# Kernel tuning notes

Hardware: AMD Instinct MI355X
Metric: run time of the kernel (lower is better)

The kernel has to match this reference:

```python
import jax, jax.numpy as jnp
import numpy as np
from jax import lax

EPS = 1e-5
GROUPS = 8
NUM_HEADS = 8


def setup_inputs() -> dict:
    key = jax.random.key(0)
    ks = jax.random.split(key, 3)
    C = 512
    x = jax.random.normal(ks[0], (8, C, 32, 32), dtype=jnp.float32)
    gamma = jnp.ones((C,), jnp.float32)
    beta = jnp.zeros((C,), jnp.float32)
    w_qkv = jax.random.normal(ks[1], (3 * C, C), dtype=jnp.float32) * (1.0 / np.sqrt(C))
    b_qkv = jnp.zeros((3 * C,), jnp.float32)
    w_proj = jax.random.normal(ks[2], (C, C), dtype=jnp.float32) * (1.0 / np.sqrt(C))
    b_proj = jnp.zeros((C,), jnp.float32)
    return {"x": x, "gamma": gamma, "beta": beta, "w_qkv": w_qkv,
            "b_qkv": b_qkv, "w_proj": w_proj, "b_proj": b_proj}


def reference(x, gamma, beta, w_qkv, b_qkv, w_proj, b_proj):
    b, c, h, w = x.shape
    hd = c // NUM_HEADS
    L = h * w
    # GroupNorm over (c/G, h, w) per group
    xg = x.reshape(b, GROUPS, c // GROUPS, h, w)
    mean = jnp.mean(xg, axis=(2, 3, 4), keepdims=True)
    var = jnp.var(xg, axis=(2, 3, 4), keepdims=True)
    xn = ((xg - mean) * lax.rsqrt(var + EPS)).reshape(b, c, h, w)
    xn = xn * gamma[None, :, None, None] + beta[None, :, None, None]
    # 1x1 conv QKV projection over flattened spatial dim
    xr = xn.reshape(b, c, L)
    qkv = jnp.einsum('oc,bcl->bol', w_qkv, xr) + b_qkv[None, :, None]
    q, k, v = jnp.split(qkv, 3, axis=1)
    # [b, H, L, hd]
    q = q.reshape(b, NUM_HEADS, hd, L).transpose(0, 1, 3, 2)
    k = k.reshape(b, NUM_HEADS, hd, L).transpose(0, 1, 3, 2)
    v = v.reshape(b, NUM_HEADS, hd, L).transpose(0, 1, 3, 2)
    scale = 1.0 / np.sqrt(hd).astype(np.float32)
    attn = jnp.einsum('bhqd,bhkd->bhqk', q, k) * scale
    attn = jax.nn.softmax(attn, axis=-1)
    out = jnp.einsum('bhqk,bhkd->bhqd', attn, v)  # [b, H, L, hd]
    out = out.transpose(0, 1, 3, 2).reshape(b, c, L)
    out = jnp.einsum('oc,bcl->bol', w_proj, out) + b_proj[None, :, None]
    return x + out.reshape(b, c, h, w)
```

## Files before the change

kernel.cpp:

```cpp
#include <hip/hip_runtime.h>
#include <hip/hip_bf16.h>

typedef unsigned short u16;
typedef __attribute__((ext_vector_type(8))) short short8;
typedef __attribute__((ext_vector_type(4))) float floatx4;
typedef __attribute__((ext_vector_type(16))) float floatx16;
typedef __attribute__((ext_vector_type(4))) unsigned uint4v;

struct __attribute__((aligned(8))) u16x4 { u16 x, y, z, w; };
struct __attribute__((aligned(16))) u16x8 { u16 v[8]; };

__device__ __forceinline__ u16 f2bf(float f) {
  unsigned u = __builtin_bit_cast(unsigned, f);
  u += 0x7fff + ((u >> 16) & 1);
  return (u16)(u >> 16);
}

__device__ __forceinline__ unsigned cvt_pk_bf16(float lo, float hi) {
  unsigned d;
  asm("v_cvt_pk_bf16_f32 %0, %1, %2" : "=v"(d) : "v"(lo), "v"(hi));
  return d;
}

__device__ __forceinline__ void gload_lds16(const u16* g, u16* l) {
  __builtin_amdgcn_global_load_lds(
      (const __attribute__((address_space(1))) void*)g,
      (__attribute__((address_space(3))) void*)l, 16, 0, 0);
}

__global__ __launch_bounds__(256) void k_convert(
    const float* __restrict__ wq, const float* __restrict__ wp,
    u16* __restrict__ oq, u16* __restrict__ op) {
  int t = blockIdx.x * 256 + threadIdx.x;
  constexpr int NQ4 = (1536 * 512) / 4;
  constexpr int NP4 = (512 * 512) / 4;
  if (t < NQ4) {
    float4 v = reinterpret_cast<const float4*>(wq)[t];
    u16x4 o = { f2bf(v.x), f2bf(v.y), f2bf(v.z), f2bf(v.w) };
    reinterpret_cast<u16x4*>(oq)[t] = o;
  } else if (t - NQ4 < NP4) {
    int i = t - NQ4;
    float4 v = reinterpret_cast<const float4*>(wp)[i];
    u16x4 o = { f2bf(v.x), f2bf(v.y), f2bf(v.z), f2bf(v.w) };
    reinterpret_cast<u16x4*>(op)[i] = o;
  }
}

__global__ __launch_bounds__(256) void k_gn_stats(const float* __restrict__ x,
                                                  float* __restrict__ stats) {
  int bg = blockIdx.x >> 3, sl = blockIdx.x & 7;
  int b = bg >> 3, g = bg & 7;
  const float* base = x + ((size_t)(b * 512 + g * 64) * 1024) + sl * 128;
  float s = 0.f, ss = 0.f;
#pragma unroll
  for (int i = 0; i < 8; ++i) {
    int idx = threadIdx.x + i * 256;
    int c = idx >> 5, l4 = idx & 31;
    float4 v = *reinterpret_cast<const float4*>(base + (size_t)c * 1024 + l4 * 4);
    s += v.x + v.y + v.z + v.w;
    ss += v.x * v.x + v.y * v.y + v.z * v.z + v.w * v.w;
  }
#pragma unroll
  for (int d = 1; d < 64; d <<= 1) { s += __shfl_xor(s, d); ss += __shfl_xor(ss, d); }
  __shared__ float rs[4], rss[4];
  int wid = threadIdx.x >> 6;
  if ((threadIdx.x & 63) == 0) { rs[wid] = s; rss[wid] = ss; }
  __syncthreads();
  if (threadIdx.x == 0) {
    stats[(bg * 8 + sl) * 2]     = rs[0] + rs[1] + rs[2] + rs[3];
    stats[(bg * 8 + sl) * 2 + 1] = rss[0] + rss[1] + rss[2] + rss[3];
  }
}

__global__ __launch_bounds__(256) void k_gn_norm(
    const float* __restrict__ x, const float* __restrict__ gamma,
    const float* __restrict__ beta, const float* __restrict__ stats,
    u16* __restrict__ xnT) {
  int bg = blockIdx.x >> 3, sl = blockIdx.x & 7;
  int b = bg >> 3, g = bg & 7;
  float s = 0.f, ss = 0.f;
#pragma unroll
  for (int i = 0; i < 8; ++i) { s += stats[(bg * 8 + i) * 2]; ss += stats[(bg * 8 + i) * 2 + 1]; }
  const float inv_n = 1.0f / 65536.0f;
  float mean = s * inv_n;
  float var = ss * inv_n - mean * mean;
  float istd = rsqrtf(var + 1e-5f);
  __shared__ float tile[128 * 65];
  const float* base = x + ((size_t)(b * 512 + g * 64) * 1024) + sl * 128;
#pragma unroll
  for (int i = 0; i < 8; ++i) {
    int idx = threadIdx.x + i * 256;
    int c = idx >> 5, l4 = idx & 31;
    float4 v = *reinterpret_cast<const float4*>(base + (size_t)c * 1024 + l4 * 4);
    float gm = gamma[g * 64 + c];
    float ga = gm * istd;
    float be = beta[g * 64 + c] - mean * ga;
    tile[(l4 * 4 + 0) * 65 + c] = v.x * ga + be;
    tile[(l4 * 4 + 1) * 65 + c] = v.y * ga + be;
    tile[(l4 * 4 + 2) * 65 + c] = v.z * ga + be;
    tile[(l4 * 4 + 3) * 65 + c] = v.w * ga + be;
  }
  __syncthreads();
  u16* obase = xnT + ((size_t)(b * 1024 + sl * 128) * 512) + g * 64;
#pragma unroll
  for (int i = 0; i < 8; ++i) {
    int idx = threadIdx.x + i * 256;
    int l = idx >> 4, c4 = (idx & 15) * 4;
    u16x4 o = { f2bf(tile[l * 65 + c4]),     f2bf(tile[l * 65 + c4 + 1]),
                f2bf(tile[l * 65 + c4 + 2]), f2bf(tile[l * 65 + c4 + 3]) };
    *reinterpret_cast<u16x4*>(obase + (size_t)l * 512 + c4) = o;
  }
}

template <int MODE>
__global__ __launch_bounds__(512) void k_gemm(
    const u16* __restrict__ A, const u16* __restrict__ Bm,
    const float* __restrict__ bias, const float* __restrict__ xres,
    u16* __restrict__ Qb, u16* __restrict__ Kb, u16* __restrict__ Vb,
    float* __restrict__ out) {
  int b = blockIdx.x & 7;
  int rem = blockIdx.x >> 3;
  int mt = rem >> 3, nt = rem & 7;
  int tid = threadIdx.x;
  int lane = tid & 63, wid = tid >> 6;
  int wm = wid >> 2, wn = wid & 3;

  union SM {
    u16 ab[2][2][128 * 64];
    u16 c16[128 * 136];
    float c32[128 * 128];
  };
  __shared__ SM sm;

  floatx4 z = {0.f, 0.f, 0.f, 0.f};
  floatx4 acc[4][2];
#pragma unroll
  for (int m = 0; m < 4; ++m)
#pragma unroll
    for (int n = 0; n < 2; ++n) acc[m][n] = z;

  const u16* Abase = A + (size_t)(mt * 128) * 512;
  const u16* Bbase = Bm + ((size_t)(b * 1024 + nt * 128)) * 512;
  int cb0 = (lane & 7) ^ (lane >> 3);
  const u16* asrc = Abase + (size_t)(wid * 16 + (lane >> 3)) * 512 + cb0 * 8;
  const u16* bsrc = Bbase + (size_t)(wid * 16 + (lane >> 3)) * 512 + cb0 * 8;

#define STAGE(BUF, KK)                                                           \
  {                                                                              \
    _Pragma("unroll")                                                            \
    for (int j = 0; j < 2; ++j) {                                                \
      gload_lds16(asrc + (size_t)j * 8 * 512 + (KK) * 64,                        \
                  &sm.ab[BUF][0][(wid * 16 + j * 8) * 64]);                      \
      gload_lds16(bsrc + (size_t)j * 8 * 512 + (KK) * 64,                        \
                  &sm.ab[BUF][1][(wid * 16 + j * 8) * 64]);                      \
    }                                                                            \
  }

  STAGE(0, 0);
#pragma unroll
  for (int kk = 0; kk < 8; ++kk) {
    const int cur = kk & 1;
    if (kk < 7) {
      STAGE(cur ^ 1, kk + 1);
      asm volatile("s_waitcnt vmcnt(4)" ::: "memory");
    } else {
      asm volatile("s_waitcnt vmcnt(0)" ::: "memory");
    }
    __builtin_amdgcn_s_barrier();
    __builtin_amdgcn_sched_barrier(0);
    const u16* Asc = sm.ab[cur][0];
    const u16* Bsc = sm.ab[cur][1];
#pragma unroll
    for (int kc = 0; kc < 2; ++kc) {
      int cbk = kc * 4 + (lane >> 4);
      short8 af[4], bf[2];
#pragma unroll
      for (int m = 0; m < 4; ++m) {
        int row = wm * 64 + m * 16 + (lane & 15);
        af[m] = *reinterpret_cast<const short8*>(Asc + row * 64 + ((cbk ^ (row & 7)) * 8));
      }
#pragma unroll
      for (int n = 0; n < 2; ++n) {
        int row = wn * 32 + n * 16 + (lane & 15);
        bf[n] = *reinterpret_cast<const short8*>(Bsc + row * 64 + ((cbk ^ (row & 7)) * 8));
      }
      __builtin_amdgcn_s_setprio(1);
#pragma unroll
      for (int m = 0; m < 4; ++m)
#pragma unroll
        for (int n = 0; n < 2; ++n)
          acc[m][n] = __builtin_amdgcn_mfma_f32_16x16x32_bf16(af[m], bf[n], acc[m][n], 0, 0, 0);
      __builtin_amdgcn_s_setprio(0);
    }
    __builtin_amdgcn_s_barrier();
  }
#undef STAGE

  int sec = (MODE == 0) ? (mt >> 2) : 0;
  int ow0 = (mt & 3) * 128;
#pragma unroll
  for (int m = 0; m < 4; ++m) {
#pragma unroll
    for (int n = 0; n < 2; ++n) {
#pragma unroll
      for (int r = 0; r < 4; ++r) {
        int o_l = wm * 64 + m * 16 + ((lane >> 4) * 4) + r;
        int l_l = wn * 32 + n * 16 + (lane & 15);
        float v = acc[m][n][r] + bias[mt * 128 + o_l];
        if (MODE == 0) {
          if (sec == 0) v *= 0.18033688f;
          u16 bv = f2bf(v);
          if (sec < 2) sm.c16[l_l * 136 + o_l] = bv;
          else         sm.c16[o_l * 136 + l_l] = bv;
        } else {
          sm.c32[o_l * 128 + l_l] = v;
        }
      }
    }
  }
  __syncthreads();
  if (MODE == 0) {
    u16* dst = (sec == 0) ? Qb : (sec == 1 ? Kb : Vb);
#pragma unroll
    for (int p = 0; p < 4; ++p) {
      int row = p * 32 + (tid >> 4);
      int col = (tid & 15) * 8;
      u16x8 vv = *reinterpret_cast<const u16x8*>(&sm.c16[row * 136 + col]);
      size_t gi;
      if (sec < 2) gi = ((size_t)(b * 1024 + nt * 128 + row)) * 512 + ow0 + col;
      else         gi = ((size_t)(b * 512 + ow0 + row)) * 1024 + nt * 128 + col;
      *reinterpret_cast<u16x8*>(dst + gi) = vv;
    }
  } else {
#pragma unroll
    for (int p = 0; p < 8; ++p) {
      int row = p * 16 + (tid >> 5);
      int col = (tid & 31) * 4;
      float4 vv = *reinterpret_cast<const float4*>(&sm.c32[row * 128 + col]);
      size_t gi = ((size_t)(b * 512 + mt * 128 + row)) * 1024 + nt * 128 + col;
      float4 xr = *reinterpret_cast<const float4*>(xres + gi);
      vv.x += xr.x; vv.y += xr.y; vv.z += xr.z; vv.w += xr.w;
      *reinterpret_cast<float4*>(out + gi) = vv;
    }
  }
}

__global__ __launch_bounds__(256) void k_attn(
    const u16* __restrict__ Qb, const u16* __restrict__ Kb,
    const u16* __restrict__ Vb, u16* __restrict__ OT) {
  int b = blockIdx.x & 7;
  int h = (blockIdx.x >> 3) & 7;
  int qt = blockIdx.x >> 6;
  int tid = threadIdx.x;
  int lane = tid & 63, wid = tid >> 6;
  int l31 = lane & 31, g = lane >> 5;
  int r7 = l31 & 7;
  __shared__ u16 Ks[64 * 64], Vs[64 * 64];

  short8 qf[4];
  int qrow = qt * 128 + wid * 32 + l31;
  const u16* qp = Qb + ((size_t)(b * 1024 + qrow)) * 512 + h * 64 + g * 8;
#pragma unroll
  for (int kc2 = 0; kc2 < 4; ++kc2)
    qf[kc2] = *reinterpret_cast<const short8*>(qp + kc2 * 16);

  floatx16 oacc[2];
#pragma unroll
  for (int nd = 0; nd < 2; ++nd)
#pragma unroll
    for (int r = 0; r < 16; ++r) oacc[nd][r] = 0.f;
  float m = -1e30f, se = 0.f;

  const u16* ksrc[2]; const u16* vsrc[2]; int sdst[2];
#pragma unroll
  for (int i = 0; i < 2; ++i) {
    int idx = tid + i * 256;
    int row = idx >> 3, cb = idx & 7;
    ksrc[i] = Kb + ((size_t)(b * 1024 + row)) * 512 + h * 64 + cb * 8;
    vsrc[i] = Vb + ((size_t)(b * 512 + h * 64 + row)) * 1024 + cb * 8;
    sdst[i] = row * 64 + ((cb ^ (row & 7)) * 8);
  }
  short8 kreg[2], vreg[2];
#pragma unroll
  for (int i = 0; i < 2; ++i) {
    kreg[i] = *reinterpret_cast<const short8*>(ksrc[i]);
    vreg[i] = *reinterpret_cast<const short8*>(vsrc[i]);
  }

  for (int kt = 0; kt < 16; ++kt) {
#pragma unroll
    for (int i = 0; i < 2; ++i) {
      *reinterpret_cast<short8*>(Ks + sdst[i]) = kreg[i];
      *reinterpret_cast<short8*>(Vs + sdst[i]) = vreg[i];
    }
    __syncthreads();
    if (kt < 15) {
#pragma unroll
      for (int i = 0; i < 2; ++i) {
        kreg[i] = *reinterpret_cast<const short8*>(ksrc[i] + (size_t)(kt + 1) * 64 * 512);
        vreg[i] = *reinterpret_cast<const short8*>(vsrc[i] + (kt + 1) * 64);
      }
    }
    floatx16 sacc[2];
#pragma unroll
    for (int nk = 0; nk < 2; ++nk)
#pragma unroll
      for (int r = 0; r < 16; ++r) sacc[nk][r] = 0.f;
#pragma unroll
    for (int nk = 0; nk < 2; ++nk) {
      const u16* krow = Ks + (nk * 32 + l31) * 64;
#pragma unroll
      for (int kc2 = 0; kc2 < 4; ++kc2) {
        int cb = kc2 * 2 + g;
        short8 kf = *reinterpret_cast<const short8*>(krow + ((cb ^ r7) * 8));
        sacc[nk] = __builtin_amdgcn_mfma_f32_32x32x16_bf16(kf, qf[kc2], sacc[nk], 0, 0, 0);
      }
    }
    float pmax = sacc[0][0];
#pragma unroll
    for (int r = 1; r < 16; ++r) pmax = fmaxf(pmax, sacc[0][r]);
#pragma unroll
    for (int r = 0; r < 16; ++r) pmax = fmaxf(pmax, sacc[1][r]);
    pmax = fmaxf(pmax, __shfl_xor(pmax, 32));
    if (__any(pmax > m + 8.0f)) {
      float mn = fmaxf(m, pmax);
      float f = __builtin_amdgcn_exp2f(m - mn);
      m = mn;
      se *= f;
#pragma unroll
      for (int nd = 0; nd < 2; ++nd)
#pragma unroll
        for (int r = 0; r < 16; ++r) oacc[nd][r] *= f;
    }
    float sum = 0.f;
#pragma unroll
    for (int nk = 0; nk < 2; ++nk)
#pragma unroll
      for (int r = 0; r < 16; ++r) {
        float pv = __builtin_amdgcn_exp2f(sacc[nk][r] - m);
        sacc[nk][r] = pv;
        sum += pv;
      }
    sum += __shfl_xor(sum, 32);
    se += sum;
#pragma unroll
    for (int nk = 0; nk < 2; ++nk) {
#pragma unroll
      for (int kc = 0; kc < 2; ++kc) {
        int base = kc * 8;
        unsigned w0 = cvt_pk_bf16(sacc[nk][base + 0], sacc[nk][base + 1]);
        unsigned w2 = cvt_pk_bf16(sacc[nk][base + 4], sacc[nk][base + 5]);
        auto s0 = __builtin_amdgcn_permlane32_swap((int)w0, (int)w2, false, false);
        unsigned w1 = cvt_pk_bf16(sacc[nk][base + 2], sacc[nk][base + 3]);
        unsigned w3 = cvt_pk_bf16(sacc[nk][base + 6], sacc[nk][base + 7]);
        auto s1 = __builtin_amdgcn_permlane32_swap((int)w1, (int)w3, false, false);
        short8 pf = __builtin_bit_cast(short8,
            uint4v{(unsigned)s0[0], (unsigned)s1[0], (unsigned)s0[1], (unsigned)s1[1]});
#pragma unroll
        for (int nd = 0; nd < 2; ++nd) {
          const u16* vrow = Vs + (nd * 32 + l31) * 64;
          int cb = nk * 4 + kc * 2 + g;
          short8 vf = *reinterpret_cast<const short8*>(vrow + ((cb ^ r7) * 8));
          oacc[nd] = __builtin_amdgcn_mfma_f32_32x32x16_bf16(vf, pf, oacc[nd], 0, 0, 0);
        }
      }
    }
    __syncthreads();
  }
  float inv = 1.0f / se;
  u16* obase = OT + ((size_t)(b * 1024 + qrow)) * 512 + h * 64;
#pragma unroll
  for (int nd = 0; nd < 2; ++nd) {
#pragma unroll
    for (int rq = 0; rq < 4; ++rq) {
      u16x4 o = { f2bf(oacc[nd][rq * 4 + 0] * inv), f2bf(oacc[nd][rq * 4 + 1] * inv),
                  f2bf(oacc[nd][rq * 4 + 2] * inv), f2bf(oacc[nd][rq * 4 + 3] * inv) };
      *reinterpret_cast<u16x4*>(obase + nd * 32 + rq * 8 + g * 4) = o;
    }
  }
}

extern "C" void kernel_launch(void* const* d_in, const int* in_sizes, int n_in,
                              void* d_out, int out_size, void* d_ws, size_t ws_size,
                              hipStream_t stream) {
  const float* x      = (const float*)d_in[0];
  const float* gamma  = (const float*)d_in[1];
  const float* beta   = (const float*)d_in[2];
  const float* w_qkv  = (const float*)d_in[3];
  const float* b_qkv  = (const float*)d_in[4];
  const float* w_proj = (const float*)d_in[5];
  const float* b_proj = (const float*)d_in[6];
  float* out = (float*)d_out;

  char* ws = (char*)d_ws;
  size_t off = 0;
  float* stats = (float*)(ws + off); off += 4096;
  u16* wqb = (u16*)(ws + off); off += (size_t)1536 * 512 * 2;
  u16* wpb = (u16*)(ws + off); off += (size_t)512 * 512 * 2;
  u16* xnT = (u16*)(ws + off); off += (size_t)8 * 1024 * 512 * 2;
  u16* Qb  = (u16*)(ws + off); off += (size_t)8 * 1024 * 512 * 2;
  u16* Kb  = (u16*)(ws + off); off += (size_t)8 * 1024 * 512 * 2;
  u16* Vb  = (u16*)(ws + off); off += (size_t)8 * 1024 * 512 * 2;
  u16* OT  = (u16*)(ws + off); off += (size_t)8 * 1024 * 512 * 2;
  if (ws_size < off) return;

  k_convert<<<1024, 256, 0, stream>>>(w_qkv, w_proj, wqb, wpb);
  k_gn_stats<<<512, 256, 0, stream>>>(x, stats);
  k_gn_norm<<<512, 256, 0, stream>>>(x, gamma, beta, stats, xnT);
  k_gemm<0><<<768, 512, 0, stream>>>(wqb, xnT, b_qkv, nullptr, Qb, Kb, Vb, nullptr);
  k_attn<<<512, 256, 0, stream>>>(Qb, Kb, Vb, OT);
  k_gemm<1><<<256, 512, 0, stream>>>(wpb, OT, b_proj, x, nullptr, nullptr, nullptr, out);
}
```

Before: 85.68 us.

## Split GEMM into dedicated QKV and proj kernels and remap block indices

Separates the templated GEMM into a QKV kernel and a projection kernel. The projection kernel now uses 256 threads with 4x4 MFMA tiles per wave, so each wave does more work per LDS read. Block index decoding in the QKV, attention and projection kernels is reordered so consecutive blocks share the same batch (and head), which is meant to improve L2 locality for shared operands. The trade-off is higher register pressure in the projection kernel and fewer waves per block.

```diff
diff --git a/kernel.cpp b/kernel.cpp
--- a/kernel.cpp
+++ b/kernel.cpp
@@ -112,15 +112,14 @@
   }
 }
 
-template <int MODE>
-__global__ __launch_bounds__(512) void k_gemm(
+__global__ __launch_bounds__(512) void k_qkv(
     const u16* __restrict__ A, const u16* __restrict__ Bm,
-    const float* __restrict__ bias, const float* __restrict__ xres,
-    u16* __restrict__ Qb, u16* __restrict__ Kb, u16* __restrict__ Vb,
-    float* __restrict__ out) {
-  int b = blockIdx.x & 7;
+    const float* __restrict__ bias,
+    u16* __restrict__ Qb, u16* __restrict__ Kb, u16* __restrict__ Vb) {
+  int nt = blockIdx.x & 7;
   int rem = blockIdx.x >> 3;
-  int mt = rem >> 3, nt = rem & 7;
+  int b = rem & 7;
+  int mt = rem >> 3;
   int tid = threadIdx.x;
   int lane = tid & 63, wid = tid >> 6;
   int wm = wid >> 2, wn = wid & 3;
@@ -128,16 +127,14 @@
   union SM {
     u16 ab[2][2][128 * 64];
     u16 c16[128 * 136];
-    float c32[128 * 128];
   };
   __shared__ SM sm;
 
-  floatx4 z = {0.f, 0.f, 0.f, 0.f};
   floatx4 acc[4][2];
 #pragma unroll
   for (int m = 0; m < 4; ++m)
 #pragma unroll
-    for (int n = 0; n < 2; ++n) acc[m][n] = z;
+    for (int n = 0; n < 2; ++n) acc[m][n] = floatx4{0.f, 0.f, 0.f, 0.f};
 
   const u16* Abase = A + (size_t)(mt * 128) * 512;
   const u16* Bbase = Bm + ((size_t)(b * 1024 + nt * 128)) * 512;
@@ -196,7 +193,7 @@
   }
 #undef STAGE
 
-  int sec = (MODE == 0) ? (mt >> 2) : 0;
+  int sec = mt >> 2;
   int ow0 = (mt & 3) * 128;
 #pragma unroll
   for (int m = 0; m < 4; ++m) {
@@ -207,50 +204,137 @@
         int o_l = wm * 64 + m * 16 + ((lane >> 4) * 4) + r;
         int l_l = wn * 32 + n * 16 + (lane & 15);
         float v = acc[m][n][r] + bias[mt * 128 + o_l];
-        if (MODE == 0) {
-          if (sec == 0) v *= 0.18033688f;
-          u16 bv = f2bf(v);
-          if (sec < 2) sm.c16[l_l * 136 + o_l] = bv;
-          else         sm.c16[o_l * 136 + l_l] = bv;
-        } else {
-          sm.c32[o_l * 128 + l_l] = v;
-        }
+        if (sec == 0) v *= 0.18033688f;
+        u16 bv = f2bf(v);
+        if (sec < 2) sm.c16[l_l * 136 + o_l] = bv;
+        else         sm.c16[o_l * 136 + l_l] = bv;
       }
     }
   }
   __syncthreads();
-  if (MODE == 0) {
-    u16* dst = (sec == 0) ? Qb : (sec == 1 ? Kb : Vb);
-#pragma unroll
-    for (int p = 0; p < 4; ++p) {
-      int row = p * 32 + (tid >> 4);
-      int col = (tid & 15) * 8;
-      u16x8 vv = *reinterpret_cast<const u16x8*>(&sm.c16[row * 136 + col]);
-      size_t gi;
-      if (sec < 2) gi = ((size_t)(b * 1024 + nt * 128 + row)) * 512 + ow0 + col;
-      else         gi = ((size_t)(b * 512 + ow0 + row)) * 1024 + nt * 128 + col;
-      *reinterpret_cast<u16x8*>(dst + gi) = vv;
-    }
-  } else {
-#pragma unroll
-    for (int p = 0; p < 8; ++p) {
-      int row = p * 16 + (tid >> 5);
-      int col = (tid & 31) * 4;
-      float4 vv = *reinterpret_cast<const float4*>(&sm.c32[row * 128 + col]);
-      size_t gi = ((size_t)(b * 512 + mt * 128 + row)) * 1024 + nt * 128 + col;
-      float4 xr = *reinterpret_cast<const float4*>(xres + gi);
-      vv.x += xr.x; vv.y += xr.y; vv.z += xr.z; vv.w += xr.w;
-      *reinterpret_cast<float4*>(out + gi) = vv;
-    }
+  u16* dst = (sec == 0) ? Qb : (sec == 1 ? Kb : Vb);
+#pragma unroll
+  for (int p = 0; p < 4; ++p) {
+    int row = p * 32 + (tid >> 4);
+    int col = (tid & 15) * 8;
+    u16x8 vv = *reinterpret_cast<const u16x8*>(&sm.c16[row * 136 + col]);
+    size_t gi;
+    if (sec < 2) gi = ((size_t)(b * 1024 + nt * 128 + row)) * 512 + ow0 + col;
+    else         gi = ((size_t)(b * 512 + ow0 + row)) * 1024 + nt * 128 + col;
+    *reinterpret_cast<u16x8*>(dst + gi) = vv;
+  }
+}
+
+__global__ __launch_bounds__(256) void k_proj(
+    const u16* __restrict__ A, const u16* __restrict__ Bm,
+    const float* __restrict__ bias, const float* __restrict__ xres,
+    float* __restrict__ out) {
+  int nt = blockIdx.x & 7;
+  int rem = blockIdx.x >> 3;
+  int b = rem & 7;
+  int mt = rem >> 3;
+  int tid = threadIdx.x;
+  int lane = tid & 63, wid = tid >> 6;
+  int wm = wid >> 1, wn = wid & 1;
+
+  union SM {
+    u16 ab[2][2][128 * 64];
+    float c32[128 * 128];
+  };
+  __shared__ SM sm;
+
+  floatx4 acc[4][4];
+#pragma unroll
+  for (int m = 0; m < 4; ++m)
+#pragma unroll
+    for (int n = 0; n < 4; ++n) acc[m][n] = floatx4{0.f, 0.f, 0.f, 0.f};
+
+  const u16* Abase = A + (size_t)(mt * 128) * 512;
+  const u16* Bbase = Bm + ((size_t)(b * 1024 + nt * 128)) * 512;
+  int cb0 = (lane & 7) ^ (lane >> 3);
+  const u16* asrc = Abase + (size_t)(wid * 32 + (lane >> 3)) * 512 + cb0 * 8;
+  const u16* bsrc = Bbase + (size_t)(wid * 32 + (lane >> 3)) * 512 + cb0 * 8;
+
+#define PSTAGE(BUF, KK)                                                          \
+  {                                                                              \
+    _Pragma("unroll")                                                            \
+    for (int j = 0; j < 4; ++j) {                                                \
+      gload_lds16(asrc + (size_t)j * 8 * 512 + (KK) * 64,                        \
+                  &sm.ab[BUF][0][(wid * 32 + j * 8) * 64]);                      \
+      gload_lds16(bsrc + (size_t)j * 8 * 512 + (KK) * 64,                        \
+                  &sm.ab[BUF][1][(wid * 32 + j * 8) * 64]);                      \
+    }                                                                            \
+  }
+
+  PSTAGE(0, 0);
+#pragma unroll
+  for (int kk = 0; kk < 8; ++kk) {
+    const int cur = kk & 1;
+    if (kk < 7) {
+      PSTAGE(cur ^ 1, kk + 1);
+      asm volatile("s_waitcnt vmcnt(8)" ::: "memory");
+    } else {
+      asm volatile("s_waitcnt vmcnt(0)" ::: "memory");
+    }
+    __builtin_amdgcn_s_barrier();
+    __builtin_amdgcn_sched_barrier(0);
+    const u16* Asc = sm.ab[cur][0];
+    const u16* Bsc = sm.ab[cur][1];
+#pragma unroll
+    for (int kc = 0; kc < 2; ++kc) {
+      int cbk = kc * 4 + (lane >> 4);
+      short8 af[4], bf[4];
+#pragma unroll
+      for (int m = 0; m < 4; ++m) {
+        int row = wm * 64 + m * 16 + (lane & 15);
+        af[m] = *reinterpret_cast<const short8*>(Asc + row * 64 + ((cbk ^ (row & 7)) * 8));
+      }
+#pragma unroll
+      for (int n = 0; n < 4; ++n) {
+        int row = wn * 64 + n * 16 + (lane & 15);
+        bf[n] = *reinterpret_cast<const short8*>(Bsc + row * 64 + ((cbk ^ (row & 7)) * 8));
+      }
+      __builtin_amdgcn_s_setprio(1);
+#pragma unroll
+      for (int m = 0; m < 4; ++m)
+#pragma unroll
+        for (int n = 0; n < 4; ++n)
+          acc[m][n] = __builtin_amdgcn_mfma_f32_16x16x32_bf16(af[m], bf[n], acc[m][n], 0, 0, 0);
+      __builtin_amdgcn_s_setprio(0);
+    }
+    __builtin_amdgcn_s_barrier();
+  }
+#undef PSTAGE
+
+#pragma unroll
+  for (int m = 0; m < 4; ++m)
+#pragma unroll
+    for (int n = 0; n < 4; ++n)
+#pragma unroll
+      for (int r = 0; r < 4; ++r) {
+        int o_l = wm * 64 + m * 16 + ((lane >> 4) * 4) + r;
+        int l_l = wn * 64 + n * 16 + (lane & 15);
+        sm.c32[o_l * 128 + l_l] = acc[m][n][r] + bias[mt * 128 + o_l];
+      }
+  __syncthreads();
+#pragma unroll
+  for (int p = 0; p < 16; ++p) {
+    int row = p * 8 + (tid >> 5);
+    int col = (tid & 31) * 4;
+    float4 vv = *reinterpret_cast<const float4*>(&sm.c32[row * 128 + col]);
+    size_t gi = ((size_t)(b * 512 + mt * 128 + row)) * 1024 + nt * 128 + col;
+    float4 xr = *reinterpret_cast<const float4*>(xres + gi);
+    vv.x += xr.x; vv.y += xr.y; vv.z += xr.z; vv.w += xr.w;
+    *reinterpret_cast<float4*>(out + gi) = vv;
   }
 }
 
 __global__ __launch_bounds__(256) void k_attn(
     const u16* __restrict__ Qb, const u16* __restrict__ Kb,
     const u16* __restrict__ Vb, u16* __restrict__ OT) {
-  int b = blockIdx.x & 7;
+  int qt = blockIdx.x & 7;
   int h = (blockIdx.x >> 3) & 7;
-  int qt = blockIdx.x >> 6;
+  int b = blockIdx.x >> 6;
   int tid = threadIdx.x;
   int lane = tid & 63, wid = tid >> 6;
   int l31 = lane & 31, g = lane >> 5;
@@ -407,7 +491,7 @@
   k_convert<<<1024, 256, 0, stream>>>(w_qkv, w_proj, wqb, wpb);
   k_gn_stats<<<512, 256, 0, stream>>>(x, stats);
   k_gn_norm<<<512, 256, 0, stream>>>(x, gamma, beta, stats, xnT);
-  k_gemm<0><<<768, 512, 0, stream>>>(wqb, xnT, b_qkv, nullptr, Qb, Kb, Vb, nullptr);
+  k_qkv<<<768, 512, 0, stream>>>(wqb, xnT, b_qkv, Qb, Kb, Vb);
   k_attn<<<512, 256, 0, stream>>>(Qb, Kb, Vb, OT);
-  k_gemm<1><<<256, 512, 0, stream>>>(wpb, OT, b_proj, x, nullptr, nullptr, nullptr, out);
-}
+  k_proj<<<256, 256, 0, stream>>>(wpb, OT, b_proj, x, out);
+}
```

After: 86.07 us. About the same (+0.5%).
